# Kernel optimization log

Measured on AMD Instinct MI355X. Metric: run time of the kernel, lower is better.

## Reference

```python
import jax, jax.numpy as jnp
import numpy as np

DIM = 512
EDIM = 2 * DIM          # edim(=2) * dim
OUT_DIM = 512
KERNEL_SIZE = 4096
B, L = 4, 4096


def setup_inputs() -> dict:
    key = jax.random.key(0)
    k0, k1, k2, k3, k4 = jax.random.split(key, 5)
    embeddings = jax.random.normal(k0, (B, L, DIM), dtype=jnp.float32)
    logit_alpha = jax.random.uniform(k1, (EDIM,), minval=-3.0, maxval=3.0, dtype=jnp.float32)
    logit_delta = jax.random.uniform(k2, (EDIM,), minval=-3.0, maxval=3.0, dtype=jnp.float32)
    # xavier_uniform: U(-a, a), a = sqrt(6/(fan_in+fan_out))
    a_beta = float(np.sqrt(6.0 / (DIM + EDIM)))
    beta = jax.random.uniform(k3, (DIM, EDIM), minval=-a_beta, maxval=a_beta, dtype=jnp.float32)
    a_eta = float(np.sqrt(6.0 / (EDIM + OUT_DIM)))
    eta = jax.random.uniform(k4, (EDIM, OUT_DIM), minval=-a_eta, maxval=a_eta, dtype=jnp.float32)
    return {"embeddings": embeddings, "logit_alpha": logit_alpha,
            "logit_delta": logit_delta, "beta": beta, "eta": eta}


def reference(embeddings, logit_alpha, logit_delta, beta, eta):
    K = KERNEL_SIZE
    Lseq = embeddings.shape[1]
    # data-dependent EMA decay kernel: kernel[e, t] = p_e * q_e^t
    alpha = jax.nn.sigmoid(logit_alpha)[:, None]            # [E, 1]
    delta = jax.nn.sigmoid(logit_delta)[:, None]            # [E, 1]
    p = alpha
    q = 1.0 - alpha * delta
    len_range = jnp.arange(K, dtype=embeddings.dtype)[None, :]   # [1, K]
    kernel = p * jnp.exp(jnp.log(q) * len_range)            # [E, K]

    u = jnp.einsum('bld,de->ble', embeddings, beta)         # [B, L, E]
    u_T = jnp.swapaxes(u, -1, -2)                           # [B, E, L]

    # forward (causal) direction: flip kernel, full conv via FFT, slice at K-1
    kernel_f = jnp.flip(kernel, axis=-1)
    fft_dim = Lseq + K
    fft_dim = 1 << (fft_dim - 1).bit_length()               # next power of 2 (static)
    inp_fft = jnp.fft.rfft(u_T, n=fft_dim, axis=-1)
    ker_fft = jnp.fft.rfft(kernel_f, n=fft_dim, axis=-1)    # [E, fft_dim//2+1]
    out_full = jnp.fft.irfft(inp_fft * ker_fft, n=fft_dim, axis=-1)
    out_T = out_full[..., K - 1:K - 1 + Lseq].astype(embeddings.dtype)  # [B, E, L]

    out = jnp.swapaxes(out_T, -1, -2)                       # [B, L, E]
    return jnp.einsum('ble,eo->blo', out, eta)              # [B, L, out_dim]
```

## Files before the change

### kernel.cpp

```cpp
#include <hip/hip_runtime.h>
#include <hip/hip_bf16.h>

#define DIM      512
#define EDIM     1024
#define OUTD     512
#define BATCH    4
#define LSEQ     4096
#define MROWS    (BATCH * LSEQ)
#define NCHUNK   64
#define CHUNK    (LSEQ / NCHUNK)

typedef __attribute__((ext_vector_type(8))) __bf16 bf16x8;
typedef __attribute__((ext_vector_type(4))) float  f32x4;

static __device__ __forceinline__ ushort f2b(float f) {
    uint x = __float_as_uint(f);
    x += 0x7fff + ((x >> 16) & 1);
    return (ushort)(x >> 16);
}
static __device__ __forceinline__ float b2f(ushort u) {
    return __uint_as_float(((uint)u) << 16);
}
static __device__ __forceinline__ float sigmoidf(float x) {
    return 1.0f / (1.0f + expf(-x));
}

__global__ void prep_cvt_kernel(const float* __restrict__ emb,
                                ushort* __restrict__ a16,
                                const float* __restrict__ beta,
                                const float* __restrict__ eta,
                                const float* __restrict__ la,
                                const float* __restrict__ ld,
                                ushort* __restrict__ betaT,
                                ushort* __restrict__ etaT,
                                float* __restrict__ p,
                                float* __restrict__ q) {
    int blk = blockIdx.x;
    if (blk < 8192) {
        int i = blk * 256 + threadIdx.x;
        float4 v = ((const float4*)emb)[i];
        ushort4 o;
        o.x = f2b(v.x); o.y = f2b(v.y); o.z = f2b(v.z); o.w = f2b(v.w);
        ((ushort4*)a16)[i] = o;
    } else {
        int i = (blk - 8192) * 256 + threadIdx.x;
        if (i < EDIM * DIM) {
            int n = i / DIM, k = i - n * DIM;
            betaT[i] = f2b(beta[(size_t)k * EDIM + n]);
        }
        if (i < OUTD * EDIM) {
            int o = i / EDIM, e = i - o * EDIM;
            etaT[i] = f2b(eta[(size_t)e * OUTD + o]);
        }
        if (i < EDIM) {
            float a = sigmoidf(la[i]);
            float d = sigmoidf(ld[i]);
            p[i] = a;
            q[i] = 1.0f - a * d;
        }
    }
}

template <int OUT_BF16, int DO_AGG>
__global__ __launch_bounds__(256) void gemm_bt(const ushort* __restrict__ A,
                                               const ushort* __restrict__ Bt,
                                               void* __restrict__ Cv,
                                               const float* __restrict__ qv,
                                               float* __restrict__ aggp,
                                               int M, int N, int K,
                                               int ncolShift) {
    __shared__ ushort smem[16384];
    const int tid  = threadIdx.x;
    const int lane = tid & 63;
    const int wid  = tid >> 6;
    const int wr   = wid >> 1, wc = wid & 1;
    const int l15  = lane & 15;
    const int l4   = lane >> 4;

    const int nwg   = gridDim.x;
    const int chunkw = nwg >> 3;
    const int flat  = (blockIdx.x & 7) * chunkw + (blockIdx.x >> 3);
    const int rowBase = (flat >> ncolShift) << 7;
    const int colBase = (flat & ((1 << ncolShift) - 1)) << 7;

    f32x4 acc[4][4] = {};

    const int nkb = K >> 6;
    for (int kb = 0; kb < nkb; ++kb) {
        #pragma unroll
        for (int r = 0; r < 4; ++r) {
            int c     = r * 256 + tid;
            int row   = c >> 3;
            int col16 = (c & 7) ^ (row & 7);
            const ushort* ga = A  + (size_t)(rowBase + row) * K + kb * 64 + col16 * 8;
            __builtin_amdgcn_global_load_lds(
                (const __attribute__((address_space(1))) void*)ga,
                (__attribute__((address_space(3))) void*)((char*)smem + c * 16),
                16, 0, 0);
            const ushort* gb = Bt + (size_t)(colBase + row) * K + kb * 64 + col16 * 8;
            __builtin_amdgcn_global_load_lds(
                (const __attribute__((address_space(1))) void*)gb,
                (__attribute__((address_space(3))) void*)((char*)smem + 16384 + c * 16),
                16, 0, 0);
        }
        __syncthreads();

        #pragma unroll
        for (int kk = 0; kk < 2; ++kk) {
            bf16x8 af[4], bfr[4];
            #pragma unroll
            for (int m = 0; m < 4; ++m) {
                int row   = wr * 64 + m * 16 + l15;
                int kbyte = kk * 64 + l4 * 16;
                int addr  = row * 128 + (kbyte ^ ((row & 7) << 4));
                af[m] = *(const bf16x8*)((const char*)smem + addr);
            }
            #pragma unroll
            for (int n = 0; n < 4; ++n) {
                int row   = wc * 64 + n * 16 + l15;
                int kbyte = kk * 64 + l4 * 16;
                int addr  = 16384 + row * 128 + (kbyte ^ ((row & 7) << 4));
                bfr[n] = *(const bf16x8*)((const char*)smem + addr);
            }
            #pragma unroll
            for (int m = 0; m < 4; ++m)
                #pragma unroll
                for (int n = 0; n < 4; ++n)
                    acc[m][n] = __builtin_amdgcn_mfma_f32_16x16x32_bf16(
                        af[m], bfr[n], acc[m][n], 0, 0, 0);
        }
        __syncthreads();
    }

    #pragma unroll
    for (int m = 0; m < 4; ++m)
        #pragma unroll
        for (int n = 0; n < 4; ++n)
            #pragma unroll
            for (int r = 0; r < 4; ++r) {
                int row = rowBase + wr * 64 + m * 16 + l4 * 4 + r;
                int col = colBase + wc * 64 + n * 16 + l15;
                if (OUT_BF16)
                    ((ushort*)Cv)[(size_t)row * N + col] = f2b(acc[m][n][r]);
                else
                    ((float*)Cv)[(size_t)row * N + col] = acc[m][n][r];
            }

    if (DO_AGG) {
        const int bidx     = rowBase >> 12;
        const int chunkIdx = ((rowBase & 4095) >> 6) + wr;
        #pragma unroll
        for (int n = 0; n < 4; ++n) {
            int col = colBase + wc * 64 + n * 16 + l15;
            float qe = qv[col];
            float q2 = qe * qe, q4 = q2 * q2, q8 = q4 * q4, q16 = q8 * q8;
            float P = 0.0f;
            #pragma unroll
            for (int m = 3; m >= 0; --m) {
                f32x4 a = acc[m][n];
                float pm = ((a[3] * qe + a[2]) * qe + a[1]) * qe + a[0];
                P = P * q16 + pm;
            }
            float ql4 = (l4 & 1 ? q4 : 1.0f) * (l4 & 2 ? q8 : 1.0f);
            P *= ql4;
            P += __shfl_xor(P, 16, 64);
            P += __shfl_xor(P, 32, 64);
            if (l4 == 0)
                aggp[(((bidx << 6) | chunkIdx) << 10) + col] = P;
        }
    }
}

__global__ void scan_apply_kernel(ushort* __restrict__ u,
                                  const float* __restrict__ pv,
                                  const float* __restrict__ qv,
                                  const float* __restrict__ agg) {
    int t = blockIdx.x * blockDim.x + threadIdx.x;
    int e0 = (t & 511) * 2;
    int c  = (t >> 9) & 63;
    int b  = t >> 15;
    float2 qe2 = *(const float2*)(qv + e0);
    float2 pe2 = *(const float2*)(pv + e0);
    float qe[2] = {qe2.x, qe2.y};
    float pe[2] = {pe2.x, pe2.y};
    float qL[2], S[2], w[2];
    #pragma unroll
    for (int k = 0; k < 2; ++k) {
        float x = qe[k];
        #pragma unroll
        for (int s = 0; s < 6; ++s) x *= x;
        qL[k] = x; S[k] = 0.0f; w[k] = 1.0f;
    }
    for (int cp = c + 1; cp < NCHUNK; ++cp) {
        float2 a = *(const float2*)(agg + (((b << 6) | cp) << 10) + e0);
        S[0] += w[0] * a.x;  w[0] *= qL[0];
        S[1] += w[1] * a.y;  w[1] *= qL[1];
    }
    ushort* up = u + ((size_t)(b * LSEQ + c * CHUNK) << 10) + e0;
    #pragma unroll 4
    for (int j = CHUNK - 1; j >= 0; --j) {
        ushort2 uv = *(ushort2*)(up + (size_t)j * EDIM);
        S[0] = b2f(uv.x) + qe[0] * S[0];
        S[1] = b2f(uv.y) + qe[1] * S[1];
        ushort2 ov;
        ov.x = f2b(pe[0] * S[0]);
        ov.y = f2b(pe[1] * S[1]);
        *(ushort2*)(up + (size_t)j * EDIM) = ov;
    }
}

extern "C" void kernel_launch(void* const* d_in, const int* in_sizes, int n_in,
                              void* d_out, int out_size, void* d_ws, size_t ws_size,
                              hipStream_t stream) {
    const float* emb  = (const float*)d_in[0];
    const float* la   = (const float*)d_in[1];
    const float* ld   = (const float*)d_in[2];
    const float* beta = (const float*)d_in[3];
    const float* eta  = (const float*)d_in[4];

    char* ws = (char*)d_ws;
    ushort* a16   = (ushort*)(ws);
    ushort* betaT = (ushort*)(ws + 16777216);
    ushort* etaT  = (ushort*)(ws + 17825792);
    ushort* u     = (ushort*)(ws + 18874368);
    float*  p     = (float*) (ws + 52428800);
    float*  q     = (float*) (ws + 52432896);
    float*  agg   = (float*) (ws + 52436992);

    prep_cvt_kernel<<<dim3(10240), dim3(256), 0, stream>>>(
        emb, a16, beta, eta, la, ld, betaT, etaT, p, q);

    gemm_bt<1, 1><<<dim3((MROWS / 128) * (EDIM / 128)), dim3(256), 0, stream>>>(
        a16, betaT, (void*)u, q, agg, MROWS, EDIM, DIM, 3);

    scan_apply_kernel<<<dim3(512), dim3(256), 0, stream>>>(u, p, q, agg);

    gemm_bt<0, 0><<<dim3((MROWS / 128) * (OUTD / 128)), dim3(256), 0, stream>>>(
        u, etaT, d_out, nullptr, nullptr, MROWS, OUTD, EDIM, 2);
}
```

Measured before the change: 87.28 us.

## Replace GEMMs with 256-row, 4-stage pipelined kernels and vectorize prep and scan

Both GEMMs move to a new 512-thread kernel with 256-row tiles, a 4-deep global-to-LDS ring buffer, explicit vmcnt waits and s_setprio around the MFMA blocks. This is meant to hide load latency and raise data reuse per tile. The weight transposes now go through 32x32 LDS tiles so global accesses are coalesced, and the scan processes 4 channels per thread. The larger tiles need up to 128KB of dynamic LDS, and each GEMM launches only 256 workgroups, which may leave some CUs idle.

```diff
diff --git a/kernel.cpp b/kernel.cpp
--- a/kernel.cpp
+++ b/kernel.cpp
@@ -35,6 +35,7 @@
                                 ushort* __restrict__ etaT,
                                 float* __restrict__ p,
                                 float* __restrict__ q) {
+    __shared__ float tf[32][33];
     int blk = blockIdx.x;
     if (blk < 8192) {
         int i = blk * 256 + threadIdx.x;
@@ -42,104 +43,146 @@
         ushort4 o;
         o.x = f2b(v.x); o.y = f2b(v.y); o.z = f2b(v.z); o.w = f2b(v.w);
         ((ushort4*)a16)[i] = o;
+    } else if (blk < 8704) {
+        int tile = blk - 8192;
+        int tr = tile >> 5, tc = tile & 31;
+        int r = threadIdx.x >> 3, c4 = (threadIdx.x & 7) * 4;
+        float4 v = *(const float4*)(beta + (size_t)(tr * 32 + r) * EDIM + tc * 32 + c4);
+        tf[r][c4 + 0] = v.x; tf[r][c4 + 1] = v.y;
+        tf[r][c4 + 2] = v.z; tf[r][c4 + 3] = v.w;
+        __syncthreads();
+        ushort4 o;
+        o.x = f2b(tf[c4 + 0][r]); o.y = f2b(tf[c4 + 1][r]);
+        o.z = f2b(tf[c4 + 2][r]); o.w = f2b(tf[c4 + 3][r]);
+        *(ushort4*)(betaT + (size_t)(tc * 32 + r) * DIM + tr * 32 + c4) = o;
+    } else if (blk < 9216) {
+        int tile = blk - 8704;
+        int tr = tile >> 4, tc = tile & 15;
+        int r = threadIdx.x >> 3, c4 = (threadIdx.x & 7) * 4;
+        float4 v = *(const float4*)(eta + (size_t)(tr * 32 + r) * OUTD + tc * 32 + c4);
+        tf[r][c4 + 0] = v.x; tf[r][c4 + 1] = v.y;
+        tf[r][c4 + 2] = v.z; tf[r][c4 + 3] = v.w;
+        __syncthreads();
+        ushort4 o;
+        o.x = f2b(tf[c4 + 0][r]); o.y = f2b(tf[c4 + 1][r]);
+        o.z = f2b(tf[c4 + 2][r]); o.w = f2b(tf[c4 + 3][r]);
+        *(ushort4*)(etaT + (size_t)(tc * 32 + r) * EDIM + tr * 32 + c4) = o;
     } else {
-        int i = (blk - 8192) * 256 + threadIdx.x;
-        if (i < EDIM * DIM) {
-            int n = i / DIM, k = i - n * DIM;
-            betaT[i] = f2b(beta[(size_t)k * EDIM + n]);
+        #pragma unroll
+        for (int j = 0; j < 4; ++j) {
+            int e = threadIdx.x * 4 + j;
+            float a = sigmoidf(la[e]);
+            float d = sigmoidf(ld[e]);
+            p[e] = a;
+            q[e] = 1.0f - a * d;
         }
-        if (i < OUTD * EDIM) {
-            int o = i / EDIM, e = i - o * EDIM;
-            etaT[i] = f2b(eta[(size_t)e * OUTD + o]);
-        }
-        if (i < EDIM) {
-            float a = sigmoidf(la[i]);
-            float d = sigmoidf(ld[i]);
-            p[i] = a;
-            q[i] = 1.0f - a * d;
-        }
-    }
-}
-
-template <int OUT_BF16, int DO_AGG>
-__global__ __launch_bounds__(256) void gemm_bt(const ushort* __restrict__ A,
-                                               const ushort* __restrict__ Bt,
-                                               void* __restrict__ Cv,
-                                               const float* __restrict__ qv,
-                                               float* __restrict__ aggp,
-                                               int M, int N, int K,
-                                               int ncolShift) {
-    __shared__ ushort smem[16384];
+    }
+}
+
+#define MFMA_BF16 __builtin_amdgcn_mfma_f32_16x16x32_bf16
+
+template <int KDIM, int BN, int NSHIFT, int OUT_BF16, int DO_AGG>
+__global__ __launch_bounds__(512, 2) void gemmr4(const ushort* __restrict__ A,
+                                                 const ushort* __restrict__ Bt,
+                                                 void* __restrict__ Cv,
+                                                 const float* __restrict__ qv,
+                                                 float* __restrict__ aggp,
+                                                 int N) {
+    constexpr int NF   = BN / 64;
+    constexpr int LB   = BN / 128;
+    constexpr int TILE = 16384 + BN * 64;
+    constexpr int NT   = KDIM / 32;
+
+    extern __shared__ __align__(16) char smem[];
     const int tid  = threadIdx.x;
     const int lane = tid & 63;
     const int wid  = tid >> 6;
-    const int wr   = wid >> 1, wc = wid & 1;
+    const int wr   = wid >> 2;
+    const int wc   = wid & 3;
     const int l15  = lane & 15;
     const int l4   = lane >> 4;
 
-    const int nwg   = gridDim.x;
-    const int chunkw = nwg >> 3;
-    const int flat  = (blockIdx.x & 7) * chunkw + (blockIdx.x >> 3);
-    const int rowBase = (flat >> ncolShift) << 7;
-    const int colBase = (flat & ((1 << ncolShift) - 1)) << 7;
-
-    f32x4 acc[4][4] = {};
-
-    const int nkb = K >> 6;
-    for (int kb = 0; kb < nkb; ++kb) {
-        #pragma unroll
-        for (int r = 0; r < 4; ++r) {
-            int c     = r * 256 + tid;
-            int row   = c >> 3;
-            int col16 = (c & 7) ^ (row & 7);
-            const ushort* ga = A  + (size_t)(rowBase + row) * K + kb * 64 + col16 * 8;
+    const int nwg  = gridDim.x;
+    const int flat = ((int)blockIdx.x & 7) * (nwg >> 3) + ((int)blockIdx.x >> 3);
+    const int rowBase = (flat >> NSHIFT) << 8;
+    const int colBase = (flat & ((1 << NSHIFT) - 1)) * BN;
+
+    const int srT = tid >> 3;
+    const int slT = (tid & 7) ^ (srT & 7);
+    const int rowT = 2 * srT + (slT >> 2);
+    const int kT   = (slT & 3) * 8;
+    const ushort* gA0 = A  + (size_t)(rowBase + rowT) * KDIM + kT;
+    const ushort* gA1 = gA0 + (size_t)128 * KDIM;
+    const ushort* gB0 = Bt + (size_t)(colBase + rowT) * KDIM + kT;
+    const ushort* gB1 = gB0 + (size_t)128 * KDIM;
+
+    const int l7 = l15 >> 1;
+    const int sx = ((((l15 & 1) * 4 + l4) ^ l7)) << 4;
+    const int aBase = (wr * 64 + l7) * 128 + sx;
+    const int bBase = 16384 + (wc * (BN / 8) + l7) * 128 + sx;
+
+    f32x4 acc[8][NF] = {};
+    bf16x8 af[8], bfr[NF];
+
+    auto ISSUE = [&](int t) {
+        const int boff = (t & 3) * TILE;
+        const size_t ko = (size_t)t * 32;
+        __builtin_amdgcn_global_load_lds(
+            (const __attribute__((address_space(1))) void*)(gA0 + ko),
+            (__attribute__((address_space(3))) void*)(smem + boff + tid * 16), 16, 0, 0);
+        __builtin_amdgcn_global_load_lds(
+            (const __attribute__((address_space(1))) void*)(gA1 + ko),
+            (__attribute__((address_space(3))) void*)(smem + boff + 8192 + tid * 16), 16, 0, 0);
+        __builtin_amdgcn_global_load_lds(
+            (const __attribute__((address_space(1))) void*)(gB0 + ko),
+            (__attribute__((address_space(3))) void*)(smem + boff + 16384 + tid * 16), 16, 0, 0);
+        if (LB == 2)
             __builtin_amdgcn_global_load_lds(
-                (const __attribute__((address_space(1))) void*)ga,
-                (__attribute__((address_space(3))) void*)((char*)smem + c * 16),
-                16, 0, 0);
-            const ushort* gb = Bt + (size_t)(colBase + row) * K + kb * 64 + col16 * 8;
-            __builtin_amdgcn_global_load_lds(
-                (const __attribute__((address_space(1))) void*)gb,
-                (__attribute__((address_space(3))) void*)((char*)smem + 16384 + c * 16),
-                16, 0, 0);
+                (const __attribute__((address_space(1))) void*)(gB1 + ko),
+                (__attribute__((address_space(3))) void*)(smem + boff + 24576 + tid * 16), 16, 0, 0);
+    };
+
+    ISSUE(0); ISSUE(1); ISSUE(2);
+    if (LB == 2) asm volatile("s_waitcnt vmcnt(8)" ::: "memory");
+    else         asm volatile("s_waitcnt vmcnt(6)" ::: "memory");
+    __builtin_amdgcn_s_barrier();
+
+    for (int t = 0; t < NT; ++t) {
+        if (t + 3 < NT) ISSUE(t + 3);
+        const char* sm = smem + (t & 3) * TILE;
+        #pragma unroll
+        for (int m = 0; m < 8; ++m)
+            af[m] = *(const bf16x8*)(sm + aBase + m * 1024);
+        #pragma unroll
+        for (int n = 0; n < NF; ++n)
+            bfr[n] = *(const bf16x8*)(sm + bBase + n * 1024);
+        __builtin_amdgcn_s_setprio(1);
+        #pragma unroll
+        for (int m = 0; m < 8; ++m)
+            #pragma unroll
+            for (int n = 0; n < NF; ++n)
+                acc[m][n] = MFMA_BF16(af[m], bfr[n], acc[m][n], 0, 0, 0);
+        __builtin_amdgcn_s_setprio(0);
+        if (t < NT - 3) {
+            if (LB == 2) asm volatile("s_waitcnt vmcnt(8)" ::: "memory");
+            else         asm volatile("s_waitcnt vmcnt(6)" ::: "memory");
+        } else if (t == NT - 3) {
+            if (LB == 2) asm volatile("s_waitcnt vmcnt(4)" ::: "memory");
+            else         asm volatile("s_waitcnt vmcnt(3)" ::: "memory");
+        } else if (t == NT - 2) {
+            asm volatile("s_waitcnt vmcnt(0)" ::: "memory");
         }
-        __syncthreads();
-
-        #pragma unroll
-        for (int kk = 0; kk < 2; ++kk) {
-            bf16x8 af[4], bfr[4];
-            #pragma unroll
-            for (int m = 0; m < 4; ++m) {
-                int row   = wr * 64 + m * 16 + l15;
-                int kbyte = kk * 64 + l4 * 16;
-                int addr  = row * 128 + (kbyte ^ ((row & 7) << 4));
-                af[m] = *(const bf16x8*)((const char*)smem + addr);
-            }
-            #pragma unroll
-            for (int n = 0; n < 4; ++n) {
-                int row   = wc * 64 + n * 16 + l15;
-                int kbyte = kk * 64 + l4 * 16;
-                int addr  = 16384 + row * 128 + (kbyte ^ ((row & 7) << 4));
-                bfr[n] = *(const bf16x8*)((const char*)smem + addr);
-            }
-            #pragma unroll
-            for (int m = 0; m < 4; ++m)
-                #pragma unroll
-                for (int n = 0; n < 4; ++n)
-                    acc[m][n] = __builtin_amdgcn_mfma_f32_16x16x32_bf16(
-                        af[m], bfr[n], acc[m][n], 0, 0, 0);
-        }
-        __syncthreads();
+        if (t < NT - 1) __builtin_amdgcn_s_barrier();
     }
 
     #pragma unroll
-    for (int m = 0; m < 4; ++m)
-        #pragma unroll
-        for (int n = 0; n < 4; ++n)
+    for (int m = 0; m < 8; ++m)
+        #pragma unroll
+        for (int n = 0; n < NF; ++n)
             #pragma unroll
             for (int r = 0; r < 4; ++r) {
-                int row = rowBase + wr * 64 + m * 16 + l4 * 4 + r;
-                int col = colBase + wc * 64 + n * 16 + l15;
+                int row = rowBase + wr * 128 + m * 16 + l4 * 4 + r;
+                int col = colBase + wc * (BN / 4) + n * 16 + l15;
                 if (OUT_BF16)
                     ((ushort*)Cv)[(size_t)row * N + col] = f2b(acc[m][n][r]);
                 else
@@ -147,26 +190,29 @@
             }
 
     if (DO_AGG) {
-        const int bidx     = rowBase >> 12;
-        const int chunkIdx = ((rowBase & 4095) >> 6) + wr;
-        #pragma unroll
-        for (int n = 0; n < 4; ++n) {
-            int col = colBase + wc * 64 + n * 16 + l15;
-            float qe = qv[col];
-            float q2 = qe * qe, q4 = q2 * q2, q8 = q4 * q4, q16 = q8 * q8;
-            float P = 0.0f;
+        const int bidx = rowBase >> 12;
+        const int chunkBase = ((rowBase & 4095) >> 6) + wr * 2;
+        #pragma unroll
+        for (int h = 0; h < 2; ++h) {
             #pragma unroll
-            for (int m = 3; m >= 0; --m) {
-                f32x4 a = acc[m][n];
-                float pm = ((a[3] * qe + a[2]) * qe + a[1]) * qe + a[0];
-                P = P * q16 + pm;
+            for (int n = 0; n < NF; ++n) {
+                int col = colBase + wc * (BN / 4) + n * 16 + l15;
+                float qe = qv[col];
+                float q2 = qe * qe, q4 = q2 * q2, q8 = q4 * q4, q16 = q8 * q8;
+                float P = 0.0f;
+                #pragma unroll
+                for (int m = 3; m >= 0; --m) {
+                    f32x4 a = acc[h * 4 + m][n];
+                    float pm = ((a[3] * qe + a[2]) * qe + a[1]) * qe + a[0];
+                    P = P * q16 + pm;
+                }
+                float ql4 = (l4 & 1 ? q4 : 1.0f) * (l4 & 2 ? q8 : 1.0f);
+                P *= ql4;
+                P += __shfl_xor(P, 16, 64);
+                P += __shfl_xor(P, 32, 64);
+                if (l4 == 0)
+                    aggp[(((bidx << 6) | (chunkBase + h)) << 10) + col] = P;
             }
-            float ql4 = (l4 & 1 ? q4 : 1.0f) * (l4 & 2 ? q8 : 1.0f);
-            P *= ql4;
-            P += __shfl_xor(P, 16, 64);
-            P += __shfl_xor(P, 32, 64);
-            if (l4 == 0)
-                aggp[(((bidx << 6) | chunkIdx) << 10) + col] = P;
         }
     }
 }
@@ -176,36 +222,38 @@
                                   const float* __restrict__ qv,
                                   const float* __restrict__ agg) {
     int t = blockIdx.x * blockDim.x + threadIdx.x;
-    int e0 = (t & 511) * 2;
-    int c  = (t >> 9) & 63;
-    int b  = t >> 15;
-    float2 qe2 = *(const float2*)(qv + e0);
-    float2 pe2 = *(const float2*)(pv + e0);
-    float qe[2] = {qe2.x, qe2.y};
-    float pe[2] = {pe2.x, pe2.y};
-    float qL[2], S[2], w[2];
+    int e0 = (t & 255) * 4;
+    int c  = (t >> 8) & 63;
+    int b  = t >> 14;
+    float4 qe4 = *(const float4*)(qv + e0);
+    float4 pe4 = *(const float4*)(pv + e0);
+    float qe[4] = {qe4.x, qe4.y, qe4.z, qe4.w};
+    float pe[4] = {pe4.x, pe4.y, pe4.z, pe4.w};
+    float qL[4], S[4], w[4];
     #pragma unroll
-    for (int k = 0; k < 2; ++k) {
+    for (int k = 0; k < 4; ++k) {
         float x = qe[k];
         #pragma unroll
         for (int s = 0; s < 6; ++s) x *= x;
         qL[k] = x; S[k] = 0.0f; w[k] = 1.0f;
     }
     for (int cp = c + 1; cp < NCHUNK; ++cp) {
-        float2 a = *(const float2*)(agg + (((b << 6) | cp) << 10) + e0);
+        float4 a = *(const float4*)(agg + (((b << 6) | cp) << 10) + e0);
         S[0] += w[0] * a.x;  w[0] *= qL[0];
         S[1] += w[1] * a.y;  w[1] *= qL[1];
+        S[2] += w[2] * a.z;  w[2] *= qL[2];
+        S[3] += w[3] * a.w;  w[3] *= qL[3];
     }
     ushort* up = u + ((size_t)(b * LSEQ + c * CHUNK) << 10) + e0;
     #pragma unroll 4
     for (int j = CHUNK - 1; j >= 0; --j) {
-        ushort2 uv = *(ushort2*)(up + (size_t)j * EDIM);
-        S[0] = b2f(uv.x) + qe[0] * S[0];
-        S[1] = b2f(uv.y) + qe[1] * S[1];
-        ushort2 ov;
-        ov.x = f2b(pe[0] * S[0]);
-        ov.y = f2b(pe[1] * S[1]);
-        *(ushort2*)(up + (size_t)j * EDIM) = ov;
+        ushort4 uv = *(ushort4*)(up + (size_t)j * EDIM);
+        ushort4 ov;
+        S[0] = b2f(uv.x) + qe[0] * S[0];  ov.x = f2b(pe[0] * S[0]);
+        S[1] = b2f(uv.y) + qe[1] * S[1];  ov.y = f2b(pe[1] * S[1]);
+        S[2] = b2f(uv.z) + qe[2] * S[2];  ov.z = f2b(pe[2] * S[2]);
+        S[3] = b2f(uv.w) + qe[3] * S[3];  ov.w = f2b(pe[3] * S[3]);
+        *(ushort4*)(up + (size_t)j * EDIM) = ov;
     }
 }
 
@@ -227,14 +275,19 @@
     float*  q     = (float*) (ws + 52432896);
     float*  agg   = (float*) (ws + 52436992);
 
-    prep_cvt_kernel<<<dim3(10240), dim3(256), 0, stream>>>(
+    (void)hipFuncSetAttribute((const void*)gemmr4<512, 256, 2, 1, 1>,
+                              hipFuncAttributeMaxDynamicSharedMemorySize, 131072);
+    (void)hipFuncSetAttribute((const void*)gemmr4<1024, 128, 2, 0, 0>,
+                              hipFuncAttributeMaxDynamicSharedMemorySize, 98304);
+
+    prep_cvt_kernel<<<dim3(9217), dim3(256), 0, stream>>>(
         emb, a16, beta, eta, la, ld, betaT, etaT, p, q);
 
-    gemm_bt<1, 1><<<dim3((MROWS / 128) * (EDIM / 128)), dim3(256), 0, stream>>>(
-        a16, betaT, (void*)u, q, agg, MROWS, EDIM, DIM, 3);
-
-    scan_apply_kernel<<<dim3(512), dim3(256), 0, stream>>>(u, p, q, agg);
-
-    gemm_bt<0, 0><<<dim3((MROWS / 128) * (OUTD / 128)), dim3(256), 0, stream>>>(
-        u, etaT, d_out, nullptr, nullptr, MROWS, OUTD, EDIM, 2);
-}
+    gemmr4<512, 256, 2, 1, 1><<<dim3(256), dim3(512), 131072, stream>>>(
+        a16, betaT, (void*)u, q, agg, EDIM);
+
+    scan_apply_kernel<<<dim3(256), dim3(256), 0, stream>>>(u, p, q, agg);
+
+    gemmr4<1024, 128, 2, 0, 0><<<dim3(256), dim3(512), 98304, stream>>>(
+        u, etaT, d_out, nullptr, nullptr, OUTD);
+}
```

After: 81.97 us. 1.06x faster.
